# Optimization experiments

Hardware: AMD Instinct MI355X
Metric: run time of the kernel (lower is better)

The kernel has to match this reference:

```python
import jax, jax.numpy as jnp
import numpy as np
from jax import lax

V, D, P, C = 151936, 1024, 64, 28
B, S = 1, 1024
EPS = 1.1920929e-07  # torch.finfo(float32).eps, used by nn.RMSNorm(eps=None)


def setup_inputs() -> dict:
    key = jax.random.key(0)
    ks = jax.random.split(key, 10)
    return {
        "tokens": jax.random.randint(ks[0], (B, S), 0, V),
        "embed_table": jax.random.normal(ks[1], (V, D), jnp.float32) * 0.02,
        "plane_proj_w": jax.random.normal(ks[2], (C, 2 * P, D), jnp.float32) * (1.0 / np.sqrt(D)),
        "back_proj_w": jax.random.normal(ks[3], (C, D, 2 * P), jnp.float32) * 0.02,
        "base_angles": jax.random.normal(ks[4], (C, P), jnp.float32) * 0.1,
        "angle_gen_w": jax.random.normal(ks[5], (P, D), jnp.float32) * 0.01,
        "scales": jnp.ones((C, D), jnp.float32),
        "shifts": jnp.zeros((C, D), jnp.float32),
        "norm_w": jnp.ones((C, D), jnp.float32),
        "decay_param": jnp.float32(0.9),
        "gate_w": jax.random.normal(ks[6], (D, D), jnp.float32) * 0.02,
        "out_norm_w": jnp.ones((D,), jnp.float32),
        "lm_head_w": jax.random.normal(ks[7], (V, D), jnp.float32) * 0.02,
    }


def _rms_norm(v, w):
    return v * lax.rsqrt(jnp.mean(v * v, axis=-1, keepdims=True) + EPS) * w


def _causal_mix(x, decay_param, gate_w):
    # state_t = d*state_{t-1} + (1-d)*x_t, causal EMA over sequence
    d = jax.nn.sigmoid(decay_param)
    def step(s, xt):
        s = d * s + (1.0 - d) * xt
        return s, s
    _, ys = lax.scan(step, jnp.zeros(x.shape[::2], x.dtype)[0:0].sum(0) + jnp.zeros((x.shape[0], x.shape[2]), x.dtype), jnp.swapaxes(x, 0, 1))
    causal = jnp.swapaxes(ys, 0, 1)  # [B,S,D]
    return x + causal @ gate_w.T


def reference(tokens, embed_table, plane_proj_w, back_proj_w, base_angles,
              angle_gen_w, scales, shifts, norm_w, decay_param, gate_w,
              out_norm_w, lm_head_w):
    x = embed_table[tokens].astype(jnp.float32)  # [B,S,D]
    n_cycles = scales.shape[0]
    for i in range(n_cycles):
        # input-dependent angle offset (detached in the original)
        extra = x.mean(axis=1) @ angle_gen_w.T          # [B,P]
        angles = base_angles[i] + lax.stop_gradient(extra.mean(axis=0)) * 0.1
        if i % 4 == 0:
            x = _causal_mix(x, decay_param, gate_w)
        # learned-plane rotation
        proj = x @ plane_proj_w[i].T                     # [B,S,2P]
        n = proj.shape[-1] // 2
        a, b = proj[..., :n], proj[..., n:]
        ca, sa = jnp.cos(angles), jnp.sin(angles)
        rot = jnp.concatenate([a * ca - b * sa, a * sa + b * ca], axis=-1)
        x_rot = x + rot @ back_proj_w[i].T
        x_act = jax.nn.silu(x_rot * scales[i] + shifts[i])
        x = x + _rms_norm(x_act - x, norm_w[i])
    x = _rms_norm(x, out_norm_w)
    return x @ lm_head_w.T  # [B,S,V]
```

## Files before the change

### kernel.cpp

```cpp
#include <hip/hip_runtime.h>

typedef __attribute__((ext_vector_type(4))) float f32x4;
typedef __attribute__((ext_vector_type(8))) short bf16x8;
typedef unsigned short u16;
typedef unsigned int u32;
typedef __attribute__((ext_vector_type(4))) unsigned short u16x4;

#define EPS 1.1920929e-07f
#define S 1024
#define D 1024
#define NV 151936
#define NCYC 28
#define SMEM_BYTES 49152

__device__ __forceinline__ u16 f2bf(float f) {
  u32 u = __float_as_uint(f);
  return (u16)((u + 0x7fffu + ((u >> 16) & 1u)) >> 16);
}
__device__ __forceinline__ float bf2f(u16 h) {
  return __uint_as_float((u32)h << 16);
}
struct bfpair { u16 h, l; };
__device__ __forceinline__ bfpair split_bf(float v) {
  bfpair r;
  r.h = f2bf(v);
  r.l = f2bf(v - bf2f(r.h));
  return r;
}

__device__ __forceinline__ void gl16(const void* g, void* s) {
  __builtin_amdgcn_global_load_lds((const __attribute__((address_space(1))) u32*)g,
                                   (__attribute__((address_space(3))) u32*)s, 16, 0, 0);
}

__device__ __forceinline__ float block_sum256(float v, float* sbuf) {
  #pragma unroll
  for (int off = 32; off; off >>= 1) v += __shfl_down(v, off);
  int lane = threadIdx.x & 63, w = threadIdx.x >> 6;
  __syncthreads();
  if (lane == 0) sbuf[w] = v;
  __syncthreads();
  return sbuf[0] + sbuf[1] + sbuf[2] + sbuf[3];
}

__global__ void k_cvt(const float* __restrict__ src, u16* __restrict__ dst, size_t n4) {
  size_t i = (size_t)blockIdx.x * 256 + threadIdx.x;
  size_t stride = (size_t)gridDim.x * 256;
  for (; i < n4; i += stride) {
    f32x4 v = ((const f32x4*)src)[i];
    u16x4 o;
    #pragma unroll
    for (int e = 0; e < 4; ++e) o[e] = f2bf(v[e]);
    ((u16x4*)dst)[i] = o;
  }
}

__global__ void k_cvt2(const float* __restrict__ src, u16* __restrict__ dh,
                       u16* __restrict__ dl, size_t n4) {
  size_t i = (size_t)blockIdx.x * 256 + threadIdx.x;
  size_t stride = (size_t)gridDim.x * 256;
  for (; i < n4; i += stride) {
    f32x4 v = ((const f32x4*)src)[i];
    u16x4 oh, ol;
    #pragma unroll
    for (int e = 0; e < 4; ++e) { bfpair p = split_bf(v[e]); oh[e] = p.h; ol[e] = p.l; }
    ((u16x4*)dh)[i] = oh;
    ((u16x4*)dl)[i] = ol;
  }
}


__device__ void gather_phase(const int* tokens, const float* embed,
                             float* x, u16* xh, u16* xl, float* cp) {
  const int t = threadIdx.x;
  if (blockIdx.x >= 256) return;
  f32x4 creg = 0.f;
  for (int rr = 0; rr < 4; ++rr) {
    int s = blockIdx.x * 4 + rr;
    int tok = tokens[s];
    f32x4 v = ((const f32x4*)(embed + (size_t)tok * D))[t];
    u16x4 oh, ol;
    #pragma unroll
    for (int e = 0; e < 4; ++e) { bfpair p = split_bf(v[e]); oh[e] = p.h; ol[e] = p.l; }
    ((f32x4*)(x + (size_t)s * D))[t] = v;
    ((u16x4*)(xh + (size_t)s * D))[t] = oh;
    ((u16x4*)(xl + (size_t)s * D))[t] = ol;
    creg += v;
  }
  *(f32x4*)(cp + (size_t)blockIdx.x * D + t * 4) = creg;
}

template <bool CADD>
__device__ void gemm64_phase(char* smem, const u16* Ah_, const u16* Al_,
                             const u16* Bh_, const u16* Bl_, int K,
                             float* xout, u16* xho, u16* xlo, float* Cout, int G) {
  const int t = threadIdx.x;
  u16* Ash = (u16*)smem;
  u16* Asl = Ash + 4096;
  u16* Bsh = Asl + 4096;
  u16* Bsl = Bsh + 4096;
  const int wave = t >> 6, lane = t & 63;
  const int fr = lane & 15, kb = lane >> 4;
  const int sr = t >> 3, skc = (t & 7) << 3;
  const int sswz = skc ^ ((sr & 7) << 3);
  for (int tile = blockIdx.x; tile < 256; tile += G) {
    const int m0 = (tile >> 4) * 64, n0 = (tile & 15) * 64;
    f32x4 acc[4];
    #pragma unroll
    for (int j = 0; j < 4; ++j) acc[j] = 0.f;

    for (int k0 = 0; k0 < K; k0 += 64) {
      #pragma unroll
      for (int it = 0; it < 2; ++it) {
        int r = it * 32 + sr;
        size_t ga = (size_t)(m0 + r) * K + k0 + sswz;
        size_t gb = (size_t)(n0 + r) * K + k0 + sswz;
        int so = r * 64 + skc;
        gl16(Ah_ + ga, Ash + so);
        gl16(Al_ + ga, Asl + so);
        gl16(Bh_ + gb, Bsh + so);
        gl16(Bl_ + gb, Bsl + so);
      }
      __syncthreads();
      #pragma unroll
      for (int ks = 0; ks < 2; ++ks) {
        const int cphys = (ks * 32 + kb * 8) ^ ((fr & 7) << 3);
        int oa = (wave * 16 + fr) * 64 + cphys;
        bf16x8 ah = *(const bf16x8*)&Ash[oa];
        bf16x8 al = *(const bf16x8*)&Asl[oa];
        #pragma unroll
        for (int j = 0; j < 4; ++j) {
          int ob = (j * 16 + fr) * 64 + cphys;
          bf16x8 bh = *(const bf16x8*)&Bsh[ob];
          bf16x8 bl = *(const bf16x8*)&Bsl[ob];
          acc[j] = __builtin_amdgcn_mfma_f32_16x16x32_bf16(ah, bh, acc[j], 0, 0, 0);
          acc[j] = __builtin_amdgcn_mfma_f32_16x16x32_bf16(ah, bl, acc[j], 0, 0, 0);
          acc[j] = __builtin_amdgcn_mfma_f32_16x16x32_bf16(al, bh, acc[j], 0, 0, 0);
        }
      }
      __syncthreads();
    }
    #pragma unroll
    for (int j = 0; j < 4; ++j)
      #pragma unroll
      for (int rg = 0; rg < 4; ++rg) {
        int m = m0 + wave * 16 + kb * 4 + rg;
        int n = n0 + j * 16 + fr;
        if (CADD) {
          float v = xout[(size_t)m * D + n] + acc[j][rg];
          xout[(size_t)m * D + n] = v;
          bfpair p = split_bf(v);
          xho[(size_t)m * D + n] = p.h;
          xlo[(size_t)m * D + n] = p.l;
        } else {
          Cout[(size_t)m * D + n] = acc[j][rg];
        }
      }
  }
}

__device__ void causal_phase(char* smem, const float* x, u16* Rh, u16* Rl,
                             float dec, int G) {
  const int t = threadIdx.x;
  for (int tile = blockIdx.x; tile < 256; tile += G) {
    int s0 = (tile >> 4) * 64, d0 = (tile & 15) * 64;
    float (*tl)[64] = (float(*)[64])smem;
    for (int idx = t; idx < 159 * 64; idx += 256) {
      int rr = idx >> 6, c = idx & 63;
      int gs = s0 - 95 + rr;
      tl[rr][c] = (gs >= 0) ? x[(size_t)gs * D + d0 + c] : 0.f;
    }
    __syncthreads();
    int c = t & 63, r0 = t >> 6;
    for (int rr = r0; rr < 64; rr += 4) {
      float acc = 0.f, w = 1.f - dec;
      int base = rr + 95;
      #pragma unroll 8
      for (int j = 0; j < 96; ++j) { acc += w * tl[base - j][c]; w *= dec; }
      bfpair p = split_bf(acc);
      Rh[(size_t)(s0 + rr) * D + d0 + c] = p.h;
      Rl[(size_t)(s0 + rr) * D + d0 + c] = p.l;
    }
    __syncthreads();
  }
}

__device__ void proj_phase(char* smem, const u16* xh, const u16* xl,
                           const u16* Bh_, const u16* Bl_, float* pacc) {
  const int t = threadIdx.x;
  const int mt = blockIdx.x & 15, kq = blockIdx.x >> 4;
  const int m0 = mt * 64;
  const int kbase = kq * 256;
  u16* Ash = (u16*)smem;
  u16* Asl = Ash + 4096;
  u16* Bsh = Asl + 4096;
  u16* Bsl = Bsh + 8192;
  const int wave = t >> 6, lane = t & 63;
  const int fr = lane & 15, kb = lane >> 4;
  const int sr = t >> 3, skc = (t & 7) << 3;
  const int sswz = skc ^ ((sr & 7) << 3);
  f32x4 acc[8];
  #pragma unroll
  for (int j = 0; j < 8; ++j) acc[j] = 0.f;

  for (int kt = 0; kt < 4; ++kt) {
    int k0 = kbase + kt * 64;
    #pragma unroll
    for (int it = 0; it < 2; ++it) {
      int r = it * 32 + sr;
      size_t ga = (size_t)(m0 + r) * D + k0 + sswz;
      gl16(xh + ga, Ash + r * 64 + skc);
      gl16(xl + ga, Asl + r * 64 + skc);
    }
    #pragma unroll
    for (int it = 0; it < 4; ++it) {
      int r = it * 32 + sr;
      size_t gb = (size_t)r * D + k0 + sswz;
      gl16(Bh_ + gb, Bsh + r * 64 + skc);
      gl16(Bl_ + gb, Bsl + r * 64 + skc);
    }
    __syncthreads();
    #pragma unroll
    for (int ks = 0; ks < 2; ++ks) {
      const int cphys = (ks * 32 + kb * 8) ^ ((fr & 7) << 3);
      int oa = (wave * 16 + fr) * 64 + cphys;
      bf16x8 ah = *(const bf16x8*)&Ash[oa];
      bf16x8 al = *(const bf16x8*)&Asl[oa];
      #pragma unroll
      for (int j = 0; j < 8; ++j) {
        int ob = (j * 16 + fr) * 64 + cphys;
        bf16x8 bh = *(const bf16x8*)&Bsh[ob];
        bf16x8 bl = *(const bf16x8*)&Bsl[ob];
        acc[j] = __builtin_amdgcn_mfma_f32_16x16x32_bf16(ah, bh, acc[j], 0, 0, 0);
        acc[j] = __builtin_amdgcn_mfma_f32_16x16x32_bf16(ah, bl, acc[j], 0, 0, 0);
        acc[j] = __builtin_amdgcn_mfma_f32_16x16x32_bf16(al, bh, acc[j], 0, 0, 0);
      }
    }
    __syncthreads();
  }
  float* pb = pacc + (size_t)blockIdx.x * 64 * 128;
  #pragma unroll
  for (int j = 0; j < 8; ++j)
    #pragma unroll
    for (int rg = 0; rg < 4; ++rg) {
      int ml = wave * 16 + kb * 4 + rg;
      pb[ml * 128 + j * 16 + fr] = acc[j][rg];
    }
}

__device__ void angles_phase(int p, const float* cp, const float* agw,
                             const float* bang_i, float* trig, float* sbuf) {
  const int t = threadIdx.x;
  float sum = 0.f;
  #pragma unroll
  for (int q = 0; q < 4; ++q) {
    int d = t + q * 256;
    float cs = 0.f;
    #pragma unroll 8
    for (int b = 0; b < 256; ++b) cs += cp[b * D + d];
    sum += cs * agw[p * D + d];
  }
  float total = block_sum256(sum, sbuf);
  if (t == 0) {
    float ang = bang_i[p] + 0.1f * (total * (1.f / (float)S));
    trig[p] = cosf(ang);
    trig[64 + p] = sinf(ang);
  }
}

__device__ void epilogue_phase(float* sbuf, float* x, u16* xh, u16* xl,
                               const float* Rf, const float* scale,
                               const float* shift, const float* nw, float* cp) {
  const int t = threadIdx.x;
  if (blockIdx.x >= 256) return;
  f32x4 sc = *(const f32x4*)(scale + t * 4);
  f32x4 sh = *(const f32x4*)(shift + t * 4);
  f32x4 nwv = *(const f32x4*)(nw + t * 4);
  f32x4 creg = 0.f;
  for (int rr = 0; rr < 4; ++rr) {
    int s = blockIdx.x * 4 + rr;
    f32x4 xv = *(const f32x4*)(x + (size_t)s * D + t * 4);
    f32x4 rv = *(const f32x4*)(Rf + (size_t)s * D + t * 4);
    float y[4], ss = 0.f;
    #pragma unroll
    for (int c = 0; c < 4; ++c) {
      float xr = xv[c] + rv[c];
      float tt = xr * sc[c] + sh[c];
      float act = tt / (1.f + expf(-tt));
      y[c] = act - xv[c];
      ss += y[c] * y[c];
    }
    float total = block_sum256(ss, sbuf);
    float inv = rsqrtf(total * (1.f / (float)D) + EPS);
    f32x4 o;
    u16x4 oh, ol;
    #pragma unroll
    for (int c = 0; c < 4; ++c) {
      o[c] = xv[c] + y[c] * inv * nwv[c];
      bfpair p = split_bf(o[c]);
      oh[c] = p.h;
      ol[c] = p.l;
      creg[c] += o[c];
    }
    *(f32x4*)(x + (size_t)s * D + t * 4) = o;
    *(u16x4*)(xh + (size_t)s * D + t * 4) = oh;
    *(u16x4*)(xl + (size_t)s * D + t * 4) = ol;
  }
  *(f32x4*)(cp + (size_t)blockIdx.x * D + t * 4) = creg;
}

__device__ void outnorm_phase(float* sbuf, const float* x, const float* w, u16* xn) {
  const int t = threadIdx.x;
  if (blockIdx.x >= 256) return;
  for (int rr = 0; rr < 4; ++rr) {
    int s = blockIdx.x * 4 + rr;
    f32x4 xv = *(const f32x4*)(x + (size_t)s * D + t * 4);
    float total = block_sum256(xv[0]*xv[0] + xv[1]*xv[1] + xv[2]*xv[2] + xv[3]*xv[3], sbuf);
    float inv = rsqrtf(total * (1.f / (float)D) + EPS);
    f32x4 wv = *(const f32x4*)(w + t * 4);
    u16x4 o;
    #pragma unroll
    for (int c = 0; c < 4; ++c) o[c] = f2bf(xv[c] * inv * wv[c]);
    *(u16x4*)(xn + (size_t)s * D + t * 4) = o;
  }
}

__global__ __launch_bounds__(256) void fb_gather(const int* tokens, const float* embed,
                                                 float* x, u16* xh, u16* xl, float* cp) {
  gather_phase(tokens, embed, x, xh, xl, cp);
}
__global__ __launch_bounds__(256) void fb_causal(const float* x, u16* Rh, u16* Rl,
                                                 const float* decay) {
  __shared__ __align__(16) char sm[40704];
  causal_phase(sm, x, Rh, Rl, 1.f / (1.f + expf(-decay[0])), gridDim.x);
}
__global__ __launch_bounds__(256) void fb_gate(const u16* Rh, const u16* Rl,
                                               const u16* gh, const u16* gl,
                                               float* x, u16* xh, u16* xl) {
  __shared__ __align__(16) char sm[32768];
  gemm64_phase<true>(sm, Rh, Rl, gh, gl, 1024, x, xh, xl, nullptr, gridDim.x);
}
__global__ __launch_bounds__(256) void fb_projang(const u16* xh, const u16* xl,
                                                  const u16* Wph, const u16* Wpl,
                                                  const float* cp, const float* agw,
                                                  const float* bang_i,
                                                  float* pacc, float* trig) {
  __shared__ __align__(16) char sm[SMEM_BYTES];
  __shared__ float sbuf[4];
  if (blockIdx.x < 64) proj_phase(sm, xh, xl, Wph, Wpl, pacc);
  else angles_phase(blockIdx.x - 64, cp, agw, bang_i, trig, sbuf);
}

__global__ __launch_bounds__(256) void fb_back(const float* __restrict__ pacc,
                                               const float* __restrict__ trig,
                                               const u16* __restrict__ Bh_,
                                               const u16* __restrict__ Bl_,
                                               float* __restrict__ Rf) {
  __shared__ u16 Ash[64 * 128];
  __shared__ u16 Asl[64 * 128];
  __shared__ u16 Bsh[64 * 64];
  __shared__ u16 Bsl[64 * 64];
  const int t = threadIdx.x;
  const int tile = blockIdx.x;
  const int mt = tile >> 4;
  const int m0 = mt * 64, n0 = (tile & 15) * 64;
  const int wave = t >> 6, lane = t & 63;
  const int fr = lane & 15, kb = lane >> 4;
  const int sr = t >> 3, skc = (t & 7) << 3;
  const int sswz = skc ^ ((sr & 7) << 3);

  #pragma unroll
  for (int ri = 0; ri < 2; ++ri) {
    int r = ri * 32 + sr;
    int pdst = skc ^ ((r & 7) << 3);
    f32x4 a0 = 0.f, a1 = 0.f, b0 = 0.f, b1 = 0.f;
    #pragma unroll
    for (int kq = 0; kq < 4; ++kq) {
      const float* pk = pacc + ((size_t)(kq * 16 + mt) * 64 + r) * 128;
      a0 += *(const f32x4*)(pk + skc);
      a1 += *(const f32x4*)(pk + skc + 4);
      b0 += *(const f32x4*)(pk + 64 + skc);
      b1 += *(const f32x4*)(pk + 64 + skc + 4);
    }
    #pragma unroll
    for (int kh = 0; kh < 2; ++kh) {
      u16 hbuf[8], lbuf[8];
      #pragma unroll
      for (int j = 0; j < 8; ++j) {
        float av = (j < 4) ? a0[j & 3] : a1[j & 3];
        float bv = (j < 4) ? b0[j & 3] : b1[j & 3];
        float ca = trig[skc + j], sa = trig[64 + skc + j];
        float v = (kh == 0) ? (av * ca - bv * sa) : (av * sa + bv * ca);
        bfpair p = split_bf(v);
        hbuf[j] = p.h;
        lbuf[j] = p.l;
      }
      int so = r * 128 + kh * 64 + pdst;
      *(bf16x8*)&Ash[so] = *(bf16x8*)hbuf;
      *(bf16x8*)&Asl[so] = *(bf16x8*)lbuf;
    }
  }
  __syncthreads();

  f32x4 acc[4];
  #pragma unroll
  for (int j = 0; j < 4; ++j) acc[j] = 0.f;

  for (int kt = 0; kt < 2; ++kt) {
    int k0 = kt * 64;
    #pragma unroll
    for (int it = 0; it < 2; ++it) {
      int r = it * 32 + sr;
      size_t gb = (size_t)(n0 + r) * 128 + k0 + sswz;
      gl16(Bh_ + gb, Bsh + r * 64 + skc);
      gl16(Bl_ + gb, Bsl + r * 64 + skc);
    }
    __syncthreads();
    #pragma unroll
    for (int ks = 0; ks < 2; ++ks) {
      const int w = (ks * 32 + kb * 8) ^ ((fr & 7) << 3);
      int oa = (wave * 16 + fr) * 128 + k0 + w;
      bf16x8 ah = *(const bf16x8*)&Ash[oa];
      bf16x8 al = *(const bf16x8*)&Asl[oa];
      #pragma unroll
      for (int j = 0; j < 4; ++j) {
        int ob = (j * 16 + fr) * 64 + w;
        bf16x8 bh = *(const bf16x8*)&Bsh[ob];
        bf16x8 bl = *(const bf16x8*)&Bsl[ob];
        acc[j] = __builtin_amdgcn_mfma_f32_16x16x32_bf16(ah, bh, acc[j], 0, 0, 0);
        acc[j] = __builtin_amdgcn_mfma_f32_16x16x32_bf16(ah, bl, acc[j], 0, 0, 0);
        acc[j] = __builtin_amdgcn_mfma_f32_16x16x32_bf16(al, bh, acc[j], 0, 0, 0);
      }
    }
    __syncthreads();
  }
  #pragma unroll
  for (int j = 0; j < 4; ++j)
    #pragma unroll
    for (int rg = 0; rg < 4; ++rg) {
      int m = m0 + wave * 16 + kb * 4 + rg;
      int n = n0 + j * 16 + fr;
      Rf[(size_t)m * D + n] = acc[j][rg];
    }
}

__global__ __launch_bounds__(256) void fb_epi(float* x, u16* xh, u16* xl, const float* Rf,
                                              const float* scale, const float* shift,
                                              const float* nw, float* cp) {
  __shared__ float sbuf[4];
  epilogue_phase(sbuf, x, xh, xl, Rf, scale, shift, nw, cp);
}
__global__ __launch_bounds__(256) void fb_outnorm(const float* x, const float* w, u16* xn) {
  __shared__ float sbuf[4];
  outnorm_phase(sbuf, x, w, xn);
}

template <bool PRECONV>
__global__ __launch_bounds__(256) void k_lm(const u16* __restrict__ A,
                                            const void* __restrict__ Wsrc,
                                            float* __restrict__ out) {
  __shared__ u16 As[128 * 64];
  __shared__ u16 Bs[128 * 64];
  const int bid = blockIdx.x;
  const int lid = (bid & 7) * 1187 + (bid >> 3);
  const int m0 = (lid & 7) * 128;
  const int n0 = (lid >> 3) * 128;
  const int t = threadIdx.x;
  const int wave = t >> 6, lane = t & 63;
  const int wm = (wave >> 1) * 64, wn = (wave & 1) * 64;
  const int fr = lane & 15, kb = lane >> 4;
  const int sr = t >> 3, skc = (t & 7) << 3;
  const int sswz = skc ^ ((sr & 7) << 3);
  const u16* Wb16 = (const u16*)Wsrc;
  const float* Wf = (const float*)Wsrc;
  f32x4 acc[4][4];
  #pragma unroll
  for (int i = 0; i < 4; ++i)
    #pragma unroll
    for (int j = 0; j < 4; ++j) acc[i][j] = 0.f;

  for (int k0 = 0; k0 < D; k0 += 64) {
    #pragma unroll
    for (int it = 0; it < 4; ++it) {
      int r = it * 32 + sr;
      gl16(A + (size_t)(m0 + r) * D + k0 + sswz, As + r * 64 + skc);
    }
    if (PRECONV) {
      #pragma unroll
      for (int it = 0; it < 4; ++it) {
        int r = it * 32 + sr;
        gl16(Wb16 + (size_t)(n0 + r) * D + k0 + sswz, Bs + r * 64 + skc);
      }
    } else {
      #pragma unroll
      for (int it = 0; it < 4; ++it) {
        int r = it * 32 + sr;
        const float* src = Wf + (size_t)(n0 + r) * D + k0 + sswz;
        f32x4 v0 = *(const f32x4*)src;
        f32x4 v1 = *(const f32x4*)(src + 4);
        u16 h[8];
        #pragma unroll
        for (int e = 0; e < 4; ++e) { h[e] = f2bf(v0[e]); h[e + 4] = f2bf(v1[e]); }
        *(bf16x8*)&Bs[r * 64 + skc] = *(bf16x8*)h;
      }
    }
    __syncthreads();
    #pragma unroll
    for (int ks = 0; ks < 2; ++ks) {
      const int cphys = (ks * 32 + kb * 8) ^ ((fr & 7) << 3);
      bf16x8 a[4], b[4];
      #pragma unroll
      for (int i = 0; i < 4; ++i) a[i] = *(const bf16x8*)&As[(wm + i * 16 + fr) * 64 + cphys];
      #pragma unroll
      for (int j = 0; j < 4; ++j) b[j] = *(const bf16x8*)&Bs[(wn + j * 16 + fr) * 64 + cphys];
      #pragma unroll
      for (int i = 0; i < 4; ++i)
        #pragma unroll
        for (int j = 0; j < 4; ++j)
          acc[i][j] = __builtin_amdgcn_mfma_f32_16x16x32_bf16(a[i], b[j], acc[i][j], 0, 0, 0);
    }
    __syncthreads();
  }
  #pragma unroll
  for (int i = 0; i < 4; ++i)
    #pragma unroll
    for (int j = 0; j < 4; ++j)
      #pragma unroll
      for (int rg = 0; rg < 4; ++rg) {
        int m = m0 + wm + i * 16 + kb * 4 + rg;
        int n = n0 + wn + j * 16 + fr;
        out[(size_t)m * NV + n] = acc[i][j][rg];
      }
}

extern "C" void kernel_launch(void* const* d_in, const int* in_sizes, int n_in,
                              void* d_out, int out_size, void* d_ws, size_t ws_size,
                              hipStream_t stream) {
  const int* tokens = (const int*)d_in[0];
  const float* embed = (const float*)d_in[1];
  const float* Wp = (const float*)d_in[2];
  const float* Wb = (const float*)d_in[3];
  const float* bang = (const float*)d_in[4];
  const float* agw = (const float*)d_in[5];
  const float* scales = (const float*)d_in[6];
  const float* shifts = (const float*)d_in[7];
  const float* normw = (const float*)d_in[8];
  const float* decay = (const float*)d_in[9];
  const float* gatew = (const float*)d_in[10];
  const float* onorm = (const float*)d_in[11];
  const float* lmw = (const float*)d_in[12];
  float* out = (float*)d_out;

  char* ws = (char*)d_ws;
  const size_t MB = 1u << 20;
  float* x = (float*)ws;
  u16* xh = (u16*)(ws + 4 * MB);
  u16* xl = (u16*)(ws + 6 * MB);
  float* Rf = (float*)(ws + 8 * MB);
  u16* Rh = (u16*)(ws + 12 * MB);
  u16* Rl = (u16*)(ws + 14 * MB);
  float* trig = (float*)(ws + 16 * MB);
  float* cp = (float*)(ws + 17 * MB);
  float* pacc = (float*)(ws + 18 * MB);
  u16* xn = (u16*)(ws + 20 * MB);
  u16* gate_h = (u16*)(ws + 22 * MB);
  u16* gate_l = (u16*)(ws + 24 * MB);
  u16* Wp_h = (u16*)(ws + 26 * MB);
  u16* Wp_l = (u16*)(ws + 33 * MB);
  u16* Wb_h = (u16*)(ws + 40 * MB);
  u16* Wb_l = (u16*)(ws + 47 * MB);
  u16* lm_bf = (u16*)(ws + 54 * MB);

  const size_t lm_elems = (size_t)NV * D;
  bool preconv = ws_size >= 54 * MB + lm_elems * 2;

  k_cvt2<<<512, 256, 0, stream>>>(gatew, gate_h, gate_l, (size_t)D * D / 4);
  k_cvt2<<<1024, 256, 0, stream>>>(Wp, Wp_h, Wp_l, (size_t)NCYC * 128 * D / 4);
  k_cvt2<<<1024, 256, 0, stream>>>(Wb, Wb_h, Wb_l, (size_t)NCYC * 128 * D / 4);
  if (preconv) k_cvt<<<2048, 256, 0, stream>>>(lmw, lm_bf, lm_elems / 4);

  fb_gather<<<256, 256, 0, stream>>>(tokens, embed, x, xh, xl, cp);
  for (int i = 0; i < NCYC; ++i) {
    const u16* Wph = Wp_h + (size_t)i * 128 * D;
    const u16* Wpl = Wp_l + (size_t)i * 128 * D;
    const u16* Wbh = Wb_h + (size_t)i * 128 * D;
    const u16* Wbl = Wb_l + (size_t)i * 128 * D;
    if ((i & 3) == 0) {
      fb_causal<<<256, 256, 0, stream>>>(x, Rh, Rl, decay);
      fb_gate<<<256, 256, 0, stream>>>(Rh, Rl, gate_h, gate_l, x, xh, xl);
    }
    fb_projang<<<128, 256, 0, stream>>>(xh, xl, Wph, Wpl, cp, agw, bang + i * 64,
                                        pacc, trig);
    fb_back<<<256, 256, 0, stream>>>(pacc, trig, Wbh, Wbl, Rf);
    fb_epi<<<256, 256, 0, stream>>>(x, xh, xl, Rf, scales + i * D, shifts + i * D,
                                    normw + i * D, cp);
  }
  fb_outnorm<<<256, 256, 0, stream>>>(x, onorm, xn);

  if (preconv)
    k_lm<true><<<9496, 256, 0, stream>>>(xn, lm_bf, out);
  else
    k_lm<false><<<9496, 256, 0, stream>>>(xn, lmw, out);
}
```

Before: 2.985 ms.

## Split projection K into 16 chunks and compute all angles in one block

The projection GEMM now uses a 16-way split-K instead of 4-way, launching 256 blocks that each handle a single 64-wide K slice, so more of the GPU is busy on this small GEMM. The 64 per-angle blocks are replaced by one block that column-sums cp once into shared memory and then computes all 64 dot products with wave reductions. In exchange, the back-projection kernel must read and sum 16 partial accumulators instead of 4, which adds global memory traffic, and the partial-sum buffer moves to a larger workspace region. That move raises the workspace size needed before the LM head weights can be pre-converted.

```diff
diff --git a/kernel.cpp b/kernel.cpp
--- a/kernel.cpp
+++ b/kernel.cpp
@@ -190,7 +190,7 @@
   const int t = threadIdx.x;
   const int mt = blockIdx.x & 15, kq = blockIdx.x >> 4;
   const int m0 = mt * 64;
-  const int kbase = kq * 256;
+  const int k0 = kq * 64;
   u16* Ash = (u16*)smem;
   u16* Asl = Ash + 4096;
   u16* Bsh = Asl + 4096;
@@ -203,40 +203,36 @@
   #pragma unroll
   for (int j = 0; j < 8; ++j) acc[j] = 0.f;
 
-  for (int kt = 0; kt < 4; ++kt) {
-    int k0 = kbase + kt * 64;
-    #pragma unroll
-    for (int it = 0; it < 2; ++it) {
-      int r = it * 32 + sr;
-      size_t ga = (size_t)(m0 + r) * D + k0 + sswz;
-      gl16(xh + ga, Ash + r * 64 + skc);
-      gl16(xl + ga, Asl + r * 64 + skc);
-    }
-    #pragma unroll
-    for (int it = 0; it < 4; ++it) {
-      int r = it * 32 + sr;
-      size_t gb = (size_t)r * D + k0 + sswz;
-      gl16(Bh_ + gb, Bsh + r * 64 + skc);
-      gl16(Bl_ + gb, Bsl + r * 64 + skc);
-    }
-    __syncthreads();
-    #pragma unroll
-    for (int ks = 0; ks < 2; ++ks) {
-      const int cphys = (ks * 32 + kb * 8) ^ ((fr & 7) << 3);
-      int oa = (wave * 16 + fr) * 64 + cphys;
-      bf16x8 ah = *(const bf16x8*)&Ash[oa];
-      bf16x8 al = *(const bf16x8*)&Asl[oa];
-      #pragma unroll
-      for (int j = 0; j < 8; ++j) {
-        int ob = (j * 16 + fr) * 64 + cphys;
-        bf16x8 bh = *(const bf16x8*)&Bsh[ob];
-        bf16x8 bl = *(const bf16x8*)&Bsl[ob];
-        acc[j] = __builtin_amdgcn_mfma_f32_16x16x32_bf16(ah, bh, acc[j], 0, 0, 0);
-        acc[j] = __builtin_amdgcn_mfma_f32_16x16x32_bf16(ah, bl, acc[j], 0, 0, 0);
-        acc[j] = __builtin_amdgcn_mfma_f32_16x16x32_bf16(al, bh, acc[j], 0, 0, 0);
-      }
-    }
-    __syncthreads();
+  #pragma unroll
+  for (int it = 0; it < 2; ++it) {
+    int r = it * 32 + sr;
+    size_t ga = (size_t)(m0 + r) * D + k0 + sswz;
+    gl16(xh + ga, Ash + r * 64 + skc);
+    gl16(xl + ga, Asl + r * 64 + skc);
+  }
+  #pragma unroll
+  for (int it = 0; it < 4; ++it) {
+    int r = it * 32 + sr;
+    size_t gb = (size_t)r * D + k0 + sswz;
+    gl16(Bh_ + gb, Bsh + r * 64 + skc);
+    gl16(Bl_ + gb, Bsl + r * 64 + skc);
+  }
+  __syncthreads();
+  #pragma unroll
+  for (int ks = 0; ks < 2; ++ks) {
+    const int cphys = (ks * 32 + kb * 8) ^ ((fr & 7) << 3);
+    int oa = (wave * 16 + fr) * 64 + cphys;
+    bf16x8 ah = *(const bf16x8*)&Ash[oa];
+    bf16x8 al = *(const bf16x8*)&Asl[oa];
+    #pragma unroll
+    for (int j = 0; j < 8; ++j) {
+      int ob = (j * 16 + fr) * 64 + cphys;
+      bf16x8 bh = *(const bf16x8*)&Bsh[ob];
+      bf16x8 bl = *(const bf16x8*)&Bsl[ob];
+      acc[j] = __builtin_amdgcn_mfma_f32_16x16x32_bf16(ah, bh, acc[j], 0, 0, 0);
+      acc[j] = __builtin_amdgcn_mfma_f32_16x16x32_bf16(ah, bl, acc[j], 0, 0, 0);
+      acc[j] = __builtin_amdgcn_mfma_f32_16x16x32_bf16(al, bh, acc[j], 0, 0, 0);
+    }
   }
   float* pb = pacc + (size_t)blockIdx.x * 64 * 128;
   #pragma unroll
@@ -248,23 +244,30 @@
     }
 }
 
-__device__ void angles_phase(int p, const float* cp, const float* agw,
-                             const float* bang_i, float* trig, float* sbuf) {
-  const int t = threadIdx.x;
-  float sum = 0.f;
-  #pragma unroll
-  for (int q = 0; q < 4; ++q) {
-    int d = t + q * 256;
-    float cs = 0.f;
-    #pragma unroll 8
-    for (int b = 0; b < 256; ++b) cs += cp[b * D + d];
-    sum += cs * agw[p * D + d];
-  }
-  float total = block_sum256(sum, sbuf);
-  if (t == 0) {
-    float ang = bang_i[p] + 0.1f * (total * (1.f / (float)S));
-    trig[p] = cosf(ang);
-    trig[64 + p] = sinf(ang);
+__device__ void angles_all(float* colsum, const float* cp, const float* agw,
+                           const float* bang_i, float* trig) {
+  const int t = threadIdx.x;
+  f32x4 acc = 0.f;
+  for (int b = 0; b < 256; ++b)
+    acc += *(const f32x4*)(cp + (size_t)b * D + t * 4);
+  *(f32x4*)&colsum[t * 4] = acc;
+  __syncthreads();
+  const int wave = t >> 6, lane = t & 63;
+  for (int pp = 0; pp < 16; ++pp) {
+    int p = wave * 16 + pp;
+    float sum = 0.f;
+    #pragma unroll
+    for (int q = 0; q < 16; ++q) {
+      int d = lane + q * 64;
+      sum += colsum[d] * agw[p * D + d];
+    }
+    #pragma unroll
+    for (int off = 32; off; off >>= 1) sum += __shfl_down(sum, off);
+    if (lane == 0) {
+      float ang = bang_i[p] + 0.1f * (sum * (1.f / (float)S));
+      trig[p] = cosf(ang);
+      trig[64 + p] = sinf(ang);
+    }
   }
 }
 
@@ -340,15 +343,14 @@
   __shared__ __align__(16) char sm[32768];
   gemm64_phase<true>(sm, Rh, Rl, gh, gl, 1024, x, xh, xl, nullptr, gridDim.x);
 }
-__global__ __launch_bounds__(256) void fb_projang(const u16* xh, const u16* xl,
-                                                  const u16* Wph, const u16* Wpl,
-                                                  const float* cp, const float* agw,
-                                                  const float* bang_i,
-                                                  float* pacc, float* trig) {
+__global__ __launch_bounds__(256) void fb_proj(const u16* xh, const u16* xl,
+                                               const u16* Wph, const u16* Wpl,
+                                               const float* cp, const float* agw,
+                                               const float* bang_i,
+                                               float* pacc, float* trig) {
   __shared__ __align__(16) char sm[SMEM_BYTES];
-  __shared__ float sbuf[4];
-  if (blockIdx.x < 64) proj_phase(sm, xh, xl, Wph, Wpl, pacc);
-  else angles_phase(blockIdx.x - 64, cp, agw, bang_i, trig, sbuf);
+  if (blockIdx.x < 256) proj_phase(sm, xh, xl, Wph, Wpl, pacc);
+  else angles_all((float*)sm, cp, agw, bang_i, trig);
 }
 
 __global__ __launch_bounds__(256) void fb_back(const float* __restrict__ pacc,
@@ -375,7 +377,7 @@
     int pdst = skc ^ ((r & 7) << 3);
     f32x4 a0 = 0.f, a1 = 0.f, b0 = 0.f, b1 = 0.f;
     #pragma unroll
-    for (int kq = 0; kq < 4; ++kq) {
+    for (int kq = 0; kq < 16; ++kq) {
       const float* pk = pacc + ((size_t)(kq * 16 + mt) * 64 + r) * 128;
       a0 += *(const f32x4*)(pk + skc);
       a1 += *(const f32x4*)(pk + skc + 4);
@@ -561,7 +563,6 @@
   u16* Rl = (u16*)(ws + 14 * MB);
   float* trig = (float*)(ws + 16 * MB);
   float* cp = (float*)(ws + 17 * MB);
-  float* pacc = (float*)(ws + 18 * MB);
   u16* xn = (u16*)(ws + 20 * MB);
   u16* gate_h = (u16*)(ws + 22 * MB);
   u16* gate_l = (u16*)(ws + 24 * MB);
@@ -569,10 +570,11 @@
   u16* Wp_l = (u16*)(ws + 33 * MB);
   u16* Wb_h = (u16*)(ws + 40 * MB);
   u16* Wb_l = (u16*)(ws + 47 * MB);
-  u16* lm_bf = (u16*)(ws + 54 * MB);
+  float* pacc = (float*)(ws + 54 * MB);
+  u16* lm_bf = (u16*)(ws + 62 * MB);
 
   const size_t lm_elems = (size_t)NV * D;
-  bool preconv = ws_size >= 54 * MB + lm_elems * 2;
+  bool preconv = ws_size >= 62 * MB + lm_elems * 2;
 
   k_cvt2<<<512, 256, 0, stream>>>(gatew, gate_h, gate_l, (size_t)D * D / 4);
   k_cvt2<<<1024, 256, 0, stream>>>(Wp, Wp_h, Wp_l, (size_t)NCYC * 128 * D / 4);
@@ -589,8 +591,8 @@
       fb_causal<<<256, 256, 0, stream>>>(x, Rh, Rl, decay);
       fb_gate<<<256, 256, 0, stream>>>(Rh, Rl, gate_h, gate_l, x, xh, xl);
     }
-    fb_projang<<<128, 256, 0, stream>>>(xh, xl, Wph, Wpl, cp, agw, bang + i * 64,
-                                        pacc, trig);
+    fb_proj<<<257, 256, 0, stream>>>(xh, xl, Wph, Wpl, cp, agw, bang + i * 64,
+                                     pacc, trig);
     fb_back<<<256, 256, 0, stream>>>(pacc, trig, Wbh, Wbl, Rf);
     fb_epi<<<256, 256, 0, stream>>>(x, xh, xl, Rf, scales + i * D, shifts + i * D,
                                     normw + i * D, cp);
```

Result: faster. 2.822 ms (-5.5%).
